# Optimization experiments

Hardware: AMD Instinct MI355X
Metric: run time of the kernel (lower is better)

## Reference

```python
import jax, jax.numpy as jnp
import numpy as np

N = 100_000      # nodes
E = 1_600_000    # edges (avg degree 16)
F = 64           # node feature dim (node_channels)
H = 64           # hidden_channels
ED = 16          # edge_embedding_size
NEG_SLOPE = 0.2


def _lin(k, fi, fo):
    return jax.random.normal(k, (fi, fo), jnp.float32) / np.sqrt(fi)


def setup_inputs() -> dict:
    key = jax.random.key(0)
    ks = jax.random.split(key, 24)
    inp = {
        "x": jax.random.normal(ks[0], (N, F), jnp.float32),
        "edge_index": jax.random.randint(ks[1], (2, E), 0, N, dtype=jnp.int64),
        "edge_attr": jax.random.normal(ks[2], (E, ED), jnp.float32),
        # conv1 (GATv2Conv -> H)
        "Wl1": _lin(ks[3], F, H), "bl1": jnp.zeros((H,), jnp.float32),
        "Wr1": _lin(ks[4], F, H), "br1": jnp.zeros((H,), jnp.float32),
        "We1": _lin(ks[5], ED, H),
        "a1": jax.random.normal(ks[6], (H,), jnp.float32) / np.sqrt(H),
        "cb1": jnp.zeros((H,), jnp.float32),
        # lin1 residual (F -> H)
        "L1w": _lin(ks[7], F, H), "L1b": jnp.zeros((H,), jnp.float32),
        # conv2 (GATv2Conv -> F)
        "Wl2": _lin(ks[8], H, F), "bl2": jnp.zeros((F,), jnp.float32),
        "Wr2": _lin(ks[9], H, F), "br2": jnp.zeros((F,), jnp.float32),
        "We2": _lin(ks[10], ED, F),
        "a2": jax.random.normal(ks[11], (F,), jnp.float32) / np.sqrt(F),
        "cb2": jnp.zeros((F,), jnp.float32),
        # lin2 residual (H -> F)
        "L2w": _lin(ks[12], H, F), "L2b": jnp.zeros((F,), jnp.float32),
    }
    return inp


def _gatv2(x, src, dst, edge_attr, Wl, bl, Wr, br, We, a, cb):
    # GATv2, heads=1, add_self_loops=False, lin_edge bias-free
    xl = x @ Wl + bl                      # [N, D] source transform (also the value)
    xr = x @ Wr + br                      # [N, D] target transform
    m = xl[src] + xr[dst] + edge_attr @ We  # [E, D]
    s = jax.nn.leaky_relu(m, NEG_SLOPE) @ a  # [E] attention logits
    smax = jax.ops.segment_max(s, dst, num_segments=N)
    ex = jnp.exp(s - smax[dst])
    den = jax.ops.segment_sum(ex, dst, num_segments=N)
    alpha = ex / (den[dst] + 1e-16)       # softmax over incoming edges per target
    out = jax.ops.segment_sum(alpha[:, None] * xl[src], dst, num_segments=N)
    return out + cb


def reference(x, edge_index, edge_attr,
              Wl1, bl1, Wr1, br1, We1, a1, cb1, L1w, L1b,
              Wl2, bl2, Wr2, br2, We2, a2, cb2, L2w, L2b):
    src, dst = edge_index[0], edge_index[1]
    h = _gatv2(x, src, dst, edge_attr, Wl1, bl1, Wr1, br1, We1, a1, cb1) + x @ L1w + L1b
    h = jax.nn.relu(h)
    out = _gatv2(h, src, dst, edge_attr, Wl2, bl2, Wr2, br2, We2, a2, cb2) + h @ L2w + L2b
    return out
```

## Files before the change

kernel.cpp:

```cpp
#include <hip/hip_runtime.h>
#include <hip/hip_fp16.h>
#include <math.h>

#define D 64
#define EDIM 16
#define NEG 0.2f
#define SCHUNK 1024
#define PAD 4

typedef _Float16 hh2 __attribute__((ext_vector_type(2)));
typedef unsigned u32x4 __attribute__((ext_vector_type(4)));
union H2cvt { unsigned u; hh2 v; __half2 h; };

#define DPP_XOR1 0xB1
#define DPP_XOR2 0x4E
#define DPP_XOR3 0x1B
template<int CTRL>
__device__ __forceinline__ float dppx(float v)
{
    return __int_as_float(__builtin_amdgcn_mov_dpp(__float_as_int(v), CTRL, 0xF, 0xF, true));
}

__global__ void node_transform(const float* __restrict__ x,
                               const float* __restrict__ Wl, const float* __restrict__ bl,
                               const float* __restrict__ Wr, const float* __restrict__ br,
                               const float* __restrict__ Lw, const float* __restrict__ Lb,
                               __half* __restrict__ xlh, float* __restrict__ xr,
                               float* __restrict__ res, int N)
{
    __shared__ float wl[D * D], wr[D * D], lw[D * D];
    for (int i = threadIdx.x; i < D * D / 4; i += blockDim.x) {
        ((float4*)wl)[i] = ((const float4*)Wl)[i];
        ((float4*)wr)[i] = ((const float4*)Wr)[i];
        ((float4*)lw)[i] = ((const float4*)Lw)[i];
    }
    int lane = threadIdx.x & 63;
    int wave = __builtin_amdgcn_readfirstlane(threadIdx.x >> 6);
    float vbl = bl[lane], vbr = br[lane], vlb = Lb[lane];
    __syncthreads();

    int gwave  = blockIdx.x * 4 + wave;
    int nwaves = gridDim.x * 4;
    for (int n0 = gwave * 8; n0 < N; n0 += nwaves * 8) {
        float al[8], ar[8], ae[8];
        #pragma unroll
        for (int j = 0; j < 8; j++) { al[j] = vbl; ar[j] = vbr; ae[j] = vlb; }

        if (n0 + 8 <= N) {
            const float* xp0 = x + (size_t)n0 * D;
            #pragma unroll 4
            for (int k = 0; k < D; k++) {
                float w1 = wl[k * D + lane];
                float w2 = wr[k * D + lane];
                float w3 = lw[k * D + lane];
                #pragma unroll
                for (int j = 0; j < 8; j++) {
                    float xv = xp0[j * D + k];
                    al[j] = fmaf(xv, w1, al[j]);
                    ar[j] = fmaf(xv, w2, ar[j]);
                    ae[j] = fmaf(xv, w3, ae[j]);
                }
            }
            #pragma unroll
            for (int j = 0; j < 8; j++) {
                int n = n0 + j;
                xlh[(size_t)n * D + lane] = __float2half(al[j]);
                xr[(size_t)n * D + lane]  = ar[j];
                res[(size_t)n * D + lane] = ae[j];
            }
        } else {
            int nr = N - n0;
            for (int k = 0; k < D; k++) {
                float w1 = wl[k * D + lane];
                float w2 = wr[k * D + lane];
                float w3 = lw[k * D + lane];
                for (int j = 0; j < nr; j++) {
                    float xv = x[(size_t)(n0 + j) * D + k];
                    al[j] = fmaf(xv, w1, al[j]);
                    ar[j] = fmaf(xv, w2, ar[j]);
                    ae[j] = fmaf(xv, w3, ae[j]);
                }
            }
            for (int j = 0; j < nr; j++) {
                int n = n0 + j;
                xlh[(size_t)n * D + lane] = __float2half(al[j]);
                xr[(size_t)n * D + lane]  = ar[j];
                res[(size_t)n * D + lane] = ae[j];
            }
        }
    }
}

__global__ void count_deg(const int* __restrict__ ei, int* __restrict__ degp,
                          int* __restrict__ rank, int E)
{
    int e = blockIdx.x * blockDim.x + threadIdx.x;
    if (e < E) rank[e] = atomicAdd(&degp[ei[E + e] << PAD], 1);
}

__global__ void scan_blocks(const int* __restrict__ degp, int* __restrict__ rowptr,
                            int* __restrict__ bsum, int N)
{
    __shared__ int tsum[256];
    int t = threadIdx.x;
    int base = blockIdx.x * SCHUNK + t * 4;
    int v0 = 0, v1 = 0, v2 = 0, v3 = 0;
    if (base + 0 < N) v0 = degp[(base + 0) << PAD];
    if (base + 1 < N) v1 = degp[(base + 1) << PAD];
    if (base + 2 < N) v2 = degp[(base + 2) << PAD];
    if (base + 3 < N) v3 = degp[(base + 3) << PAD];
    int local = v0 + v1 + v2 + v3;
    tsum[t] = local;
    __syncthreads();
    for (int off = 1; off < 256; off <<= 1) {
        int x = (t >= off) ? tsum[t - off] : 0;
        __syncthreads();
        tsum[t] += x;
        __syncthreads();
    }
    int excl = tsum[t] - local;
    if (base + 0 < N) rowptr[base + 0] = excl;
    if (base + 1 < N) rowptr[base + 1] = excl + v0;
    if (base + 2 < N) rowptr[base + 2] = excl + v0 + v1;
    if (base + 3 < N) rowptr[base + 3] = excl + v0 + v1 + v2;
    if (t == 0) bsum[blockIdx.x] = tsum[255];
}

__global__ void scan_bsums(int* __restrict__ bsum, int nb, int* __restrict__ rowptrN)
{
    __shared__ int part[256];
    int t = threadIdx.x;
    int C = (nb + 255) / 256;
    int b = t * C, e = min(b + C, nb);
    int sum = 0;
    for (int i = b; i < e; i++) sum += bsum[i];
    part[t] = sum;
    __syncthreads();
    for (int off = 1; off < 256; off <<= 1) {
        int x = (t >= off) ? part[t - off] : 0;
        __syncthreads();
        part[t] += x;
        __syncthreads();
    }
    int running = part[t] - sum;
    for (int i = b; i < e; i++) {
        int v = bsum[i];
        bsum[i] = running;
        running += v;
    }
    if (t == 255) *rowptrN = part[255];
}

__global__ void add_offsets(int* __restrict__ rowptr, const int* __restrict__ bsum, int N)
{
    int i = blockIdx.x * blockDim.x + threadIdx.x;
    if (i < N) rowptr[i] += bsum[i >> 10];
}

__global__ void scatter_edges(const int* __restrict__ ei, const float* __restrict__ eattr,
                              const int* __restrict__ rowptr, const int* __restrict__ rank,
                              int* __restrict__ esrc, __half* __restrict__ eah, int E)
{
    int e = blockIdx.x * blockDim.x + threadIdx.x;
    if (e >= E) return;
    int dst = ei[E + e];
    int pos = rowptr[dst] + rank[e];
    esrc[pos] = ei[e];
    const float4* s4 = (const float4*)(eattr + (size_t)e * EDIM);
    float4 f0 = s4[0], f1 = s4[1], f2 = s4[2], f3 = s4[3];
    H2cvt c;
    unsigned w[8];
    c.h = __floats2half2_rn(f0.x, f0.y); w[0] = c.u;
    c.h = __floats2half2_rn(f0.z, f0.w); w[1] = c.u;
    c.h = __floats2half2_rn(f1.x, f1.y); w[2] = c.u;
    c.h = __floats2half2_rn(f1.z, f1.w); w[3] = c.u;
    c.h = __floats2half2_rn(f2.x, f2.y); w[4] = c.u;
    c.h = __floats2half2_rn(f2.z, f2.w); w[5] = c.u;
    c.h = __floats2half2_rn(f3.x, f3.y); w[6] = c.u;
    c.h = __floats2half2_rn(f3.z, f3.w); w[7] = c.u;
    u32x4* d4 = (u32x4*)(eah + (size_t)pos * EDIM);
    d4[0] = (u32x4){w[0], w[1], w[2], w[3]};
    d4[1] = (u32x4){w[4], w[5], w[6], w[7]};
}

__device__ __forceinline__ float bpx(float v, int addr)
{
    return __int_as_float(__builtin_amdgcn_ds_bpermute(addr, __float_as_int(v)));
}

__device__ __forceinline__ float edge_dot(const __half* __restrict__ eah, int ee,
                                          const hh2* w2)
{
    const unsigned* ea = (const unsigned*)(eah + (size_t)ee * EDIM);
    float acc = 0.f;
    #pragma unroll
    for (int k = 0; k < 8; k++) {
        H2cvt c; c.u = ea[k];
#if defined(__has_builtin) && __has_builtin(__builtin_amdgcn_fdot2)
        acc = __builtin_amdgcn_fdot2(c.v, w2[k], acc, false);
#else
        acc += (float)(c.v[0] * w2[k][0]) + (float)(c.v[1] * w2[k][1]);
#endif
    }
    return acc;
}

__global__ void __launch_bounds__(64) gat_fused(
                          const int* __restrict__ rowptr, const int* __restrict__ esrc,
                          const __half* __restrict__ eah,
                          const float* __restrict__ We, const float* __restrict__ avec,
                          const __half* __restrict__ xlh, const float* __restrict__ xr,
                          const float* __restrict__ res, const float* __restrict__ cb,
                          float* __restrict__ out, int N, int do_relu)
{
    int wid = __builtin_amdgcn_readfirstlane(blockIdx.x);
    int lane = threadIdx.x & 63;
    if (wid >= N) return;

    hh2 w2[8];
    #pragma unroll
    for (int j = 0; j < 8; j++) {
        H2cvt c;
        c.h = __floats2half2_rn(We[(2 * j) * D + lane], We[(2 * j + 1) * D + lane]);
        w2[j] = c.v;
    }
    float av  = avec[lane];
    float xrv = xr[(size_t)wid * D + lane];
    int beg = __builtin_amdgcn_readfirstlane(rowptr[wid]);
    int end = __builtin_amdgcn_readfirstlane(rowptr[wid + 1]);

    const int la4 = lane << 2;
    const int A4 = la4 ^ 16, A8 = la4 ^ 32, A16 = la4 ^ 64, A32 = la4 ^ 128;
    int c0 = lane & 1, c1 = lane & 2;

    float S4 = 0.f, Sr = 0.f, O = 0.f;
    int e = beg;
    for (; e + 8 <= end; e += 8) {
        float pA[4], xA[4], pB[4], xB[4];
        #pragma unroll
        for (int j = 0; j < 4; j++) {
            int s = __builtin_amdgcn_readfirstlane(esrc[e + j]);
            xA[j] = __half2float(xlh[(size_t)s * D + lane]);
            float ew = edge_dot(eah, e + j, w2);
            float m = xA[j] + xrv + ew;
            pA[j] = fmaf(NEG, fminf(m, 0.f), fmaxf(m, 0.f)) * av;
        }
        #pragma unroll
        for (int j = 0; j < 4; j++) {
            int s = __builtin_amdgcn_readfirstlane(esrc[e + 4 + j]);
            xB[j] = __half2float(xlh[(size_t)s * D + lane]);
            float ew = edge_dot(eah, e + 4 + j, w2);
            float m = xB[j] + xrv + ew;
            pB[j] = fmaf(NEG, fminf(m, 0.f), fmaxf(m, 0.f)) * av;
        }
        #pragma unroll
        for (int j = 0; j < 4; j++) { pA[j] += dppx<DPP_XOR1>(pA[j]); pB[j] += dppx<DPP_XOR1>(pB[j]); }
        #pragma unroll
        for (int j = 0; j < 4; j++) { pA[j] += dppx<DPP_XOR2>(pA[j]); pB[j] += dppx<DPP_XOR2>(pB[j]); }
        float vA = c1 ? (c0 ? pA[3] : pA[2]) : (c0 ? pA[1] : pA[0]);
        float vB = c1 ? (c0 ? pB[3] : pB[2]) : (c0 ? pB[1] : pB[0]);
        vA += bpx(vA, A4);  vB += bpx(vB, A4);
        vA += bpx(vA, A8);  vB += bpx(vB, A8);
        vA += bpx(vA, A16); vB += bpx(vB, A16);
        vA += bpx(vA, A32); vB += bpx(vB, A32);
        float evA = __expf(vA), evB = __expf(vB);
        S4 += evA; S4 += evB;
        float qA1 = dppx<DPP_XOR1>(evA), qB1 = dppx<DPP_XOR1>(evB);
        float qA2 = dppx<DPP_XOR2>(evA), qB2 = dppx<DPP_XOR2>(evB);
        float qA3 = dppx<DPP_XOR3>(evA), qB3 = dppx<DPP_XOR3>(evB);
        float y0a = c0 ? xA[1] : xA[0], y0b = c0 ? xA[3] : xA[2];
        float y1a = c0 ? xA[0] : xA[1], y1b = c0 ? xA[2] : xA[3];
        float xcA  = c1 ? y0b : y0a, xc1A = c1 ? y1b : y1a;
        float xc2A = c1 ? y0a : y0b, xc3A = c1 ? y1a : y1b;
        O = fmaf(evA, xcA, fmaf(qA1, xc1A, fmaf(qA2, xc2A, fmaf(qA3, xc3A, O))));
        float z0a = c0 ? xB[1] : xB[0], z0b = c0 ? xB[3] : xB[2];
        float z1a = c0 ? xB[0] : xB[1], z1b = c0 ? xB[2] : xB[3];
        float xcB  = c1 ? z0b : z0a, xc1B = c1 ? z1b : z1a;
        float xc2B = c1 ? z0a : z0b, xc3B = c1 ? z1a : z1b;
        O = fmaf(evB, xcB, fmaf(qB1, xc1B, fmaf(qB2, xc2B, fmaf(qB3, xc3B, O))));
    }
    for (; e + 4 <= end; e += 4) {
        float pp[4], xlv[4];
        #pragma unroll
        for (int j = 0; j < 4; j++) {
            int s = __builtin_amdgcn_readfirstlane(esrc[e + j]);
            xlv[j] = __half2float(xlh[(size_t)s * D + lane]);
            float ew = edge_dot(eah, e + j, w2);
            float m = xlv[j] + xrv + ew;
            pp[j] = fmaf(NEG, fminf(m, 0.f), fmaxf(m, 0.f)) * av;
        }
        #pragma unroll
        for (int j = 0; j < 4; j++) pp[j] += dppx<DPP_XOR1>(pp[j]);
        #pragma unroll
        for (int j = 0; j < 4; j++) pp[j] += dppx<DPP_XOR2>(pp[j]);
        float t0 = c0 ? pp[1] : pp[0];
        float t1 = c0 ? pp[3] : pp[2];
        float v  = c1 ? t1 : t0;
        v += bpx(v, A4); v += bpx(v, A8); v += bpx(v, A16); v += bpx(v, A32);
        float ev = __expf(v);
        S4 += ev;
        float q1 = dppx<DPP_XOR1>(ev);
        float q2 = dppx<DPP_XOR2>(ev);
        float q3 = dppx<DPP_XOR3>(ev);
        float y0a = c0 ? xlv[1] : xlv[0], y0b = c0 ? xlv[3] : xlv[2];
        float y1a = c0 ? xlv[0] : xlv[1], y1b = c0 ? xlv[2] : xlv[3];
        float x_c  = c1 ? y0b : y0a;
        float x_c1 = c1 ? y1b : y1a;
        float x_c2 = c1 ? y0a : y0b;
        float x_c3 = c1 ? y1a : y1b;
        O = fmaf(ev, x_c, fmaf(q1, x_c1, fmaf(q2, x_c2, fmaf(q3, x_c3, O))));
    }
    for (; e < end; ++e) {
        int s = __builtin_amdgcn_readfirstlane(esrc[e]);
        float xlv = __half2float(xlh[(size_t)s * D + lane]);
        float ew = edge_dot(eah, e, w2);
        float m = xlv + xrv + ew;
        float p = fmaf(NEG, fminf(m, 0.f), fmaxf(m, 0.f)) * av;
        p += dppx<DPP_XOR1>(p); p += dppx<DPP_XOR2>(p);
        p += bpx(p, A4); p += bpx(p, A8); p += bpx(p, A16); p += bpx(p, A32);
        float w = __expf(p);
        Sr += w;
        O = fmaf(w, xlv, O);
    }
    S4 += dppx<DPP_XOR1>(S4);
    S4 += dppx<DPP_XOR2>(S4);
    float S = S4 + Sr;

    float v = O / (S + 1e-16f) + cb[lane] + res[(size_t)wid * D + lane];
    if (do_relu) v = fmaxf(v, 0.f);
    out[(size_t)wid * D + lane] = v;
}

extern "C" void kernel_launch(void* const* d_in, const int* in_sizes, int n_in,
                              void* d_out, int out_size, void* d_ws, size_t ws_size,
                              hipStream_t stream)
{
    const float* x     = (const float*)d_in[0];
    const int*   ei    = (const int*)d_in[1];
    const float* eattr = (const float*)d_in[2];
    const float* Wl1 = (const float*)d_in[3];  const float* bl1 = (const float*)d_in[4];
    const float* Wr1 = (const float*)d_in[5];  const float* br1 = (const float*)d_in[6];
    const float* We1 = (const float*)d_in[7];  const float* a1  = (const float*)d_in[8];
    const float* cb1 = (const float*)d_in[9];
    const float* L1w = (const float*)d_in[10]; const float* L1b = (const float*)d_in[11];
    const float* Wl2 = (const float*)d_in[12]; const float* bl2 = (const float*)d_in[13];
    const float* Wr2 = (const float*)d_in[14]; const float* br2 = (const float*)d_in[15];
    const float* We2 = (const float*)d_in[16]; const float* a2  = (const float*)d_in[17];
    const float* cb2 = (const float*)d_in[18];
    const float* L2w = (const float*)d_in[19]; const float* L2b = (const float*)d_in[20];

    const int N = in_sizes[0] / D;
    const int E = in_sizes[1] / 2;
    const int NB = (N + SCHUNK - 1) / SCHUNK;

    char* wsb = (char*)d_ws;
    float*  xr   = (float*)wsb;  wsb += (size_t)N * D * sizeof(float);
    float*  res  = (float*)wsb;  wsb += (size_t)N * D * sizeof(float);
    __half* xlh  = (__half*)wsb; wsb += (size_t)N * D * sizeof(__half);
    __half* eah  = (__half*)wsb; wsb += (size_t)E * EDIM * sizeof(__half);
    int* esrc    = (int*)wsb;    wsb += (size_t)E * sizeof(int);
    int* rowptr  = (int*)wsb;    wsb += (size_t)(N + 1) * sizeof(int);
    int* bsum    = (int*)wsb;    wsb += (size_t)NB * sizeof(int);
    int* degp    = (int*)res;
    int* rank    = (int*)xlh;

    float* out = (float*)d_out;

    const int et = (E + 255) / 256;

    hipMemsetAsync(degp, 0, ((size_t)N << PAD) * sizeof(int), stream);
    count_deg<<<et, 256, 0, stream>>>(ei, degp, rank, E);
    scan_blocks<<<NB, 256, 0, stream>>>(degp, rowptr, bsum, N);
    scan_bsums<<<1, 256, 0, stream>>>(bsum, NB, rowptr + N);
    add_offsets<<<(N + 255) / 256, 256, 0, stream>>>(rowptr, bsum, N);
    scatter_edges<<<et, 256, 0, stream>>>(ei, eattr, rowptr, rank, esrc, eah, E);

    node_transform<<<1024, 256, 0, stream>>>(x, Wl1, bl1, Wr1, br1, L1w, L1b,
                                             xlh, xr, res, N);
    gat_fused<<<N, 64, 0, stream>>>(rowptr, esrc, eah, We1, a1,
                                    xlh, xr, res, cb1, out, N, 1);

    node_transform<<<1024, 256, 0, stream>>>(out, Wl2, bl2, Wr2, br2, L2w, L2b,
                                             xlh, xr, res, N);
    gat_fused<<<N, 64, 0, stream>>>(rowptr, esrc, eah, We2, a2,
                                    xlh, xr, res, cb2, out, N, 0);
}
```

Measured before the change: 452.7 us.

## Fuse first node transform with degree counting in one launch

Merges the first layer's node_transform and the count_deg atomic histogram into a single kernel whose trailing blocks do edge counting (unrolled 8 edges per thread), so the compute-heavy transform overlaps with the atomic-bound counting. degp and rank get dedicated workspace buffers instead of aliasing res/xlh, which is what lets the two run concurrently. Weights are now read straight from global memory (cached) instead of being staged in LDS. The extra workspace use and L1/L2-served weight loads may cost some bandwidth.

```diff
diff --git a/kernel.cpp b/kernel.cpp
--- a/kernel.cpp
+++ b/kernel.cpp
@@ -7,6 +7,8 @@
 #define NEG 0.2f
 #define SCHUNK 1024
 #define PAD 4
+#define NT_BLOCKS 1024
+#define CUNROLL 8
 
 typedef _Float16 hh2 __attribute__((ext_vector_type(2)));
 typedef unsigned u32x4 __attribute__((ext_vector_type(4)));
@@ -21,26 +23,15 @@
     return __int_as_float(__builtin_amdgcn_mov_dpp(__float_as_int(v), CTRL, 0xF, 0xF, true));
 }
 
-__global__ void node_transform(const float* __restrict__ x,
-                               const float* __restrict__ Wl, const float* __restrict__ bl,
-                               const float* __restrict__ Wr, const float* __restrict__ br,
-                               const float* __restrict__ Lw, const float* __restrict__ Lb,
-                               __half* __restrict__ xlh, float* __restrict__ xr,
-                               float* __restrict__ res, int N)
-{
-    __shared__ float wl[D * D], wr[D * D], lw[D * D];
-    for (int i = threadIdx.x; i < D * D / 4; i += blockDim.x) {
-        ((float4*)wl)[i] = ((const float4*)Wl)[i];
-        ((float4*)wr)[i] = ((const float4*)Wr)[i];
-        ((float4*)lw)[i] = ((const float4*)Lw)[i];
-    }
-    int lane = threadIdx.x & 63;
-    int wave = __builtin_amdgcn_readfirstlane(threadIdx.x >> 6);
+__device__ __forceinline__ void nt_body(const float* __restrict__ x,
+                                        const float* __restrict__ Wl, const float* __restrict__ bl,
+                                        const float* __restrict__ Wr, const float* __restrict__ br,
+                                        const float* __restrict__ Lw, const float* __restrict__ Lb,
+                                        __half* __restrict__ xlh, float* __restrict__ xr,
+                                        float* __restrict__ res, int N,
+                                        int gwave, int nwaves, int lane)
+{
     float vbl = bl[lane], vbr = br[lane], vlb = Lb[lane];
-    __syncthreads();
-
-    int gwave  = blockIdx.x * 4 + wave;
-    int nwaves = gridDim.x * 4;
     for (int n0 = gwave * 8; n0 < N; n0 += nwaves * 8) {
         float al[8], ar[8], ae[8];
         #pragma unroll
@@ -50,9 +41,9 @@
             const float* xp0 = x + (size_t)n0 * D;
             #pragma unroll 4
             for (int k = 0; k < D; k++) {
-                float w1 = wl[k * D + lane];
-                float w2 = wr[k * D + lane];
-                float w3 = lw[k * D + lane];
+                float w1 = Wl[k * D + lane];
+                float w2 = Wr[k * D + lane];
+                float w3 = Lw[k * D + lane];
                 #pragma unroll
                 for (int j = 0; j < 8; j++) {
                     float xv = xp0[j * D + k];
@@ -71,9 +62,9 @@
         } else {
             int nr = N - n0;
             for (int k = 0; k < D; k++) {
-                float w1 = wl[k * D + lane];
-                float w2 = wr[k * D + lane];
-                float w3 = lw[k * D + lane];
+                float w1 = Wl[k * D + lane];
+                float w2 = Wr[k * D + lane];
+                float w3 = Lw[k * D + lane];
                 for (int j = 0; j < nr; j++) {
                     float xv = x[(size_t)(n0 + j) * D + k];
                     al[j] = fmaf(xv, w1, al[j]);
@@ -91,11 +82,41 @@
     }
 }
 
-__global__ void count_deg(const int* __restrict__ ei, int* __restrict__ degp,
-                          int* __restrict__ rank, int E)
-{
-    int e = blockIdx.x * blockDim.x + threadIdx.x;
-    if (e < E) rank[e] = atomicAdd(&degp[ei[E + e] << PAD], 1);
+__global__ void nt_and_count(const float* __restrict__ x,
+                             const float* __restrict__ Wl, const float* __restrict__ bl,
+                             const float* __restrict__ Wr, const float* __restrict__ br,
+                             const float* __restrict__ Lw, const float* __restrict__ Lb,
+                             __half* __restrict__ xlh, float* __restrict__ xr,
+                             float* __restrict__ res, int N,
+                             const int* __restrict__ ei, int* __restrict__ degp,
+                             int* __restrict__ rank, int E)
+{
+    if (blockIdx.x >= NT_BLOCKS) {
+        int bb = (blockIdx.x - NT_BLOCKS) * (blockDim.x * CUNROLL) + threadIdx.x;
+        #pragma unroll
+        for (int j = 0; j < CUNROLL; j++) {
+            int e = bb + j * blockDim.x;
+            if (e < E) rank[e] = atomicAdd(&degp[ei[E + e] << PAD], 1);
+        }
+        return;
+    }
+    int lane = threadIdx.x & 63;
+    int wave = __builtin_amdgcn_readfirstlane(threadIdx.x >> 6);
+    nt_body(x, Wl, bl, Wr, br, Lw, Lb, xlh, xr, res, N,
+            blockIdx.x * 4 + wave, NT_BLOCKS * 4, lane);
+}
+
+__global__ void node_transform(const float* __restrict__ x,
+                               const float* __restrict__ Wl, const float* __restrict__ bl,
+                               const float* __restrict__ Wr, const float* __restrict__ br,
+                               const float* __restrict__ Lw, const float* __restrict__ Lb,
+                               __half* __restrict__ xlh, float* __restrict__ xr,
+                               float* __restrict__ res, int N)
+{
+    int lane = threadIdx.x & 63;
+    int wave = __builtin_amdgcn_readfirstlane(threadIdx.x >> 6);
+    nt_body(x, Wl, bl, Wr, br, Lw, Lb, xlh, xr, res, N,
+            blockIdx.x * 4 + wave, gridDim.x * 4, lane);
 }
 
 __global__ void scan_blocks(const int* __restrict__ degp, int* __restrict__ rowptr,
@@ -361,22 +382,24 @@
     int* esrc    = (int*)wsb;    wsb += (size_t)E * sizeof(int);
     int* rowptr  = (int*)wsb;    wsb += (size_t)(N + 1) * sizeof(int);
     int* bsum    = (int*)wsb;    wsb += (size_t)NB * sizeof(int);
-    int* degp    = (int*)res;
-    int* rank    = (int*)xlh;
+    int* degp    = (int*)wsb;    wsb += ((size_t)N << PAD) * sizeof(int);
+    int* rank    = (int*)wsb;    wsb += (size_t)E * sizeof(int);
 
     float* out = (float*)d_out;
 
     const int et = (E + 255) / 256;
+    const int cb_blocks = (E + 256 * CUNROLL - 1) / (256 * CUNROLL);
 
     hipMemsetAsync(degp, 0, ((size_t)N << PAD) * sizeof(int), stream);
-    count_deg<<<et, 256, 0, stream>>>(ei, degp, rank, E);
+    nt_and_count<<<NT_BLOCKS + cb_blocks, 256, 0, stream>>>(
+        x, Wl1, bl1, Wr1, br1, L1w, L1b, xlh, xr, res, N,
+        ei, degp, rank, E);
+
     scan_blocks<<<NB, 256, 0, stream>>>(degp, rowptr, bsum, N);
     scan_bsums<<<1, 256, 0, stream>>>(bsum, NB, rowptr + N);
     add_offsets<<<(N + 255) / 256, 256, 0, stream>>>(rowptr, bsum, N);
     scatter_edges<<<et, 256, 0, stream>>>(ei, eattr, rowptr, rank, esrc, eah, E);
 
-    node_transform<<<1024, 256, 0, stream>>>(x, Wl1, bl1, Wr1, br1, L1w, L1b,
-                                             xlh, xr, res, N);
     gat_fused<<<N, 64, 0, stream>>>(rowptr, esrc, eah, We1, a1,
                                     xlh, xr, res, cb1, out, N, 1);
 
```

New measurement: 429.7 us (median of 2 runs). 1.05x faster.
